# Kernel tuning notes

Hardware: AMD Instinct MI355X
Metric: run time of the kernel (lower is better)

The kernel has to match this reference:

```python
import jax, jax.numpy as jnp
import numpy as np

N_FRAG = 1_000_000
CELL_N = 1000
GENE_N = 500
N_GENES = 5000
H = 100   # hidden dims
E = 100   # embedding dims


def setup_inputs() -> dict:
    key = jax.random.key(0)
    ks = jax.random.split(key, 16)
    coords = jax.random.randint(ks[0], (N_FRAG, 2), 0, 1000, dtype=jnp.int64 if jax.config.jax_enable_x64 else jnp.int32)
    cxg_ix = jnp.sort(jax.random.randint(ks[1], (N_FRAG,), 0, CELL_N * GENE_N))
    gene_ix = jax.random.randint(ks[2], (GENE_N,), 0, N_GENES)
    stdv_in = 1.0 / np.sqrt(2)
    stdv_h = 1.0 / np.sqrt(H)
    u = lambda k, shape, s: jax.random.uniform(k, shape, jnp.float32, -s, s)
    W0 = u(ks[3], (2, H), stdv_in); b0 = u(ks[4], (H,), stdv_in)
    W1 = u(ks[5], (H, H), stdv_h); b1 = u(ks[6], (H,), stdv_h)
    W2 = u(ks[7], (H, H), stdv_h); b2 = u(ks[8], (H,), stdv_h)
    W3 = u(ks[9], (H, E), stdv_h); b3 = u(ks[10], (E,), stdv_h)
    weight1 = u(ks[11], (N_GENES, E), stdv_h / 100.0)  # torch init: stdv/100
    bias1 = jax.random.normal(ks[12], (N_GENES,), jnp.float32)  # mean gene expression
    return {
        "fragment_coordinates": coords,
        "fragment_cellxgene_ix": cxg_ix,
        "cell_n": CELL_N,
        "gene_n": GENE_N,
        "gene_ix": gene_ix,
        "W0": W0, "b0": b0, "W1": W1, "b1": b1,
        "W2": W2, "b2": b2, "W3": W3, "b3": b3,
        "weight1": weight1, "bias1": bias1,
    }


def reference(fragment_coordinates, fragment_cellxgene_ix, cell_n, gene_n, gene_ix,
              W0, b0, W1, b1, W2, b2, W3, b3, weight1, bias1):
    # FragmentEmbedder: 4-layer MLP on scaled coordinates
    x = fragment_coordinates.astype(jnp.float32) / 1000.0          # [F, 2]
    h = jax.nn.relu(x @ W0 + b0)
    h = jax.nn.relu(h @ W1 + b1)
    h = jax.nn.relu(h @ W2 + b2)
    emb = h @ W3 + b3                                              # [F, E]
    # EmbeddingGenePooler: segment-sum into cell x gene bins
    pooled = jax.ops.segment_sum(emb, fragment_cellxgene_ix,
                                 num_segments=cell_n * gene_n)     # [C*G, E]
    cg = pooled.reshape(cell_n, gene_n, -1)                        # [C, G, E]
    # EmbeddingToExpression: gene-specific weighted sum + bias
    out = jnp.einsum('cge,ge->cg', cg, weight1[gene_ix]) + bias1[gene_ix]
    return out
```

## Files before the change

kernel.cpp:

```cpp
#include <hip/hip_runtime.h>
#include <hip/hip_bf16.h>

typedef __attribute__((ext_vector_type(4))) short s16x4;
typedef __attribute__((ext_vector_type(4))) float f32x4;

#define GENE_N     500
#define WG_STRIDE  112
#define WSW_FRAGS  154
#define WG_OFF_BYTES 81920

__device__ __forceinline__ unsigned short f2bf(float x){
  __hip_bfloat16 h = __float2bfloat16(x);
  return *reinterpret_cast<unsigned short*>(&h);
}

__device__ __forceinline__ f32x4 mfma16(s16x4 a, s16x4 b, f32x4 c){
#if __has_builtin(__builtin_amdgcn_mfma_f32_16x16x16bf16_1k)
  return __builtin_amdgcn_mfma_f32_16x16x16bf16_1k(a, b, c, 0, 0, 0);
#else
  asm volatile("v_mfma_f32_16x16x16_bf16 %0, %1, %2, %0"
               : "+v"(c) : "v"(a), "v"(b));
  return c;
#endif
}

__global__ void init_out(const int* __restrict__ gene_ix,
                         const float* __restrict__ bias1,
                         float* __restrict__ out, int n){
  int t = blockIdx.x*blockDim.x + threadIdx.x;
  if (t < n) out[t] = bias1[gene_ix[t % GENE_N]];
}

__global__ void prep_weights(const float* __restrict__ W0, const float* __restrict__ b0,
                             const float* __restrict__ W1, const float* __restrict__ b1,
                             const float* __restrict__ W2, const float* __restrict__ b2,
                             const float* __restrict__ W3, const float* __restrict__ b3,
                             unsigned short* __restrict__ wsW){
  int t = blockIdx.x*blockDim.x + threadIdx.x;
  if (t >= WSW_FRAGS*64) return;
  int fr = t >> 6, lane = t & 63;
  int grp = lane >> 4, row = lane & 15;
  int L, m, kt;
  if (fr < 7){ L = 0; m = fr; kt = 0; }
  else { int r = fr - 7; L = 1 + r/49; r %= 49; m = r/7; kt = r%7; }
  int up = m*16 + row;
  const float* W = (L==0)?W0:(L==1)?W1:(L==2)?W2:W3;
  const float* B = (L==0)?b0:(L==1)?b1:(L==2)?b2:b3;
  #pragma unroll
  for (int i = 0; i < 4; ++i){
    float val = 0.f;
    if (up < 100){
      int k = kt*16 + grp*4 + i;
      if (L == 0){
        if (k < 2)        val = W[k*100 + up];
        else if (k == 2)  val = B[up];
      } else {
        if (k < 100)      val = W[k*100 + up];
        else if (k == 100) val = B[up];
      }
    }
    wsW[t*4 + i] = f2bf(val);
  }
}

__global__ void prep_wg(const int* __restrict__ gene_ix,
                        const float* __restrict__ weight1,
                        float* __restrict__ wg){
  int t = blockIdx.x*blockDim.x + threadIdx.x;
  if (t >= GENE_N*WG_STRIDE) return;
  int g = t / WG_STRIDE, e = t % WG_STRIDE;
  wg[t] = (e < 100) ? weight1[gene_ix[g]*100 + e] : 0.f;
}


__device__ __forceinline__ void mfma_layer(const s16x4* __restrict__ A,
                                           const s16x4* __restrict__ g,
                                           f32x4* __restrict__ acc){
  const f32x4 zero = {0.f,0.f,0.f,0.f};
  #pragma unroll
  for (int m = 0; m < 7; ++m){
    f32x4 a = zero;
    #pragma unroll
    for (int kt = 0; kt < 7; ++kt) a = mfma16(A[m*7 + kt], g[kt], a);
    acc[m] = a;
  }
}

__device__ __forceinline__ void pack_relu(const f32x4* __restrict__ acc,
                                          s16x4* __restrict__ g, int grp){
  #pragma unroll
  for (int m = 0; m < 7; ++m){
    float r0 = fmaxf(acc[m][0], 0.f);
    float r1 = fmaxf(acc[m][1], 0.f);
    float r2 = fmaxf(acc[m][2], 0.f);
    float r3 = fmaxf(acc[m][3], 0.f);
    if (m == 6 && grp == 1) r0 = 1.0f;
    s16x4 v;
    v[0] = (short)f2bf(r0);
    v[1] = (short)f2bf(r1);
    v[2] = (short)f2bf(r2);
    v[3] = (short)f2bf(r3);
    g[m] = v;
  }
}

__device__ __forceinline__ void epi_store(const f32x4* __restrict__ acc,
                                          const float* __restrict__ wg,
                                          int grp, int lane, int f, int nfrag,
                                          int cxgv, float* __restrict__ out){
  int gbin = cxgv % GENE_N;
  const float* wrow = wg + gbin*WG_STRIDE + grp*4;
  float s = 0.f;
  #pragma unroll
  for (int m = 0; m < 7; ++m){
    float4 w = *(const float4*)(wrow + m*16);
    s += acc[m][0]*w.x + acc[m][1]*w.y + acc[m][2]*w.z + acc[m][3]*w.w;
  }
  s += __shfl_xor(s, 16);
  s += __shfl_xor(s, 32);
  if (lane < 16 && f < nfrag) atomicAdd(out + cxgv, s);
}

__device__ __forceinline__ s16x4 build_bx(int2 cd){
  s16x4 v;
  v[0] = (short)f2bf((float)cd.x * 1e-3f);
  v[1] = (short)f2bf((float)cd.y * 1e-3f);
  v[2] = (short)0x3F80;
  v[3] = 0;
  return v;
}

__global__ __launch_bounds__(64, 1)
void frag_mlp_pool(const int* __restrict__ coords, const int* __restrict__ cxg,
                   const unsigned short* __restrict__ wsW,
                   const float* __restrict__ wg,
                   float* __restrict__ out, int nfrag, int ntiles){
  const int lane = threadIdx.x & 63;
  const int grp = lane >> 4, row = lane & 15;
  const s16x4* wf = (const s16x4*)wsW;

  s16x4 A0[7], A1[49], A2[49], A3[49];
  #pragma unroll
  for (int i = 0; i < 7;  ++i) A0[i] = wf[i*64 + lane];
  #pragma unroll
  for (int i = 0; i < 49; ++i) A1[i] = wf[(7   + i)*64 + lane];
  #pragma unroll
  for (int i = 0; i < 49; ++i) A2[i] = wf[(56  + i)*64 + lane];
  #pragma unroll
  for (int i = 0; i < 49; ++i) A3[i] = wf[(105 + i)*64 + lane];

  const f32x4 zero = {0.f,0.f,0.f,0.f};
  const int npairs = (ntiles + 1) >> 1;
  const int lastf = nfrag - 1;

  int p0 = blockIdx.x;
  int fA = p0*32 + row, fB = p0*32 + 16 + row;
  int cA = (fA < nfrag) ? fA : lastf;
  int cB = (fB < nfrag) ? fB : lastf;
  int2 cdA = ((const int2*)coords)[cA];
  int2 cdB = ((const int2*)coords)[cB];
  int  xgA = cxg[cA];
  int  xgB = cxg[cB];

  for (int p = p0; p < npairs; p += gridDim.x){
    int f0 = p*32 + row, f1 = p*32 + 16 + row;
    int2 cd0 = cdA, cd1 = cdB;
    int  xg0 = xgA, xg1 = xgB;

    int pn = p + gridDim.x;
    int fAn = pn*32 + row, fBn = pn*32 + 16 + row;
    int cAn = (fAn < nfrag) ? fAn : lastf;
    int cBn = (fBn < nfrag) ? fBn : lastf;
    cdA = ((const int2*)coords)[cAn];
    cdB = ((const int2*)coords)[cBn];
    xgA = cxg[cAn];
    xgB = cxg[cBn];

    s16x4 bx0 = build_bx(cd0);
    s16x4 bx1 = build_bx(cd1);
    f32x4 acc0[7], acc1[7];
    #pragma unroll
    for (int m = 0; m < 7; ++m) acc0[m] = mfma16(A0[m], bx0, zero);
    #pragma unroll
    for (int m = 0; m < 7; ++m) acc1[m] = mfma16(A0[m], bx1, zero);

    s16x4 g0[7], g1[7];
    pack_relu(acc0, g0, grp);
    mfma_layer(A1, g0, acc0);   pack_relu(acc1, g1, grp);
    mfma_layer(A1, g1, acc1);   pack_relu(acc0, g0, grp);
    mfma_layer(A2, g0, acc0);   pack_relu(acc1, g1, grp);
    mfma_layer(A2, g1, acc1);   pack_relu(acc0, g0, grp);
    mfma_layer(A3, g0, acc0);   pack_relu(acc1, g1, grp);
    mfma_layer(A3, g1, acc1);

    epi_store(acc0, wg, grp, lane, f0, nfrag, xg0, out);
    epi_store(acc1, wg, grp, lane, f1, nfrag, xg1, out);
  }
}

extern "C" void kernel_launch(void* const* d_in, const int* in_sizes, int n_in,
                              void* d_out, int out_size, void* d_ws, size_t ws_size,
                              hipStream_t stream){
  const int* coords  = (const int*)d_in[0];
  const int* cxg     = (const int*)d_in[1];
  const int* gene_ix = (const int*)d_in[4];
  const float* W0 = (const float*)d_in[5];
  const float* b0 = (const float*)d_in[6];
  const float* W1 = (const float*)d_in[7];
  const float* b1 = (const float*)d_in[8];
  const float* W2 = (const float*)d_in[9];
  const float* b2 = (const float*)d_in[10];
  const float* W3 = (const float*)d_in[11];
  const float* b3 = (const float*)d_in[12];
  const float* weight1 = (const float*)d_in[13];
  const float* bias1   = (const float*)d_in[14];

  int nfrag  = in_sizes[1];
  int ntiles = (nfrag + 15) / 16;

  unsigned short* wsW = (unsigned short*)d_ws;
  float* wg = (float*)((char*)d_ws + WG_OFF_BYTES);
  float* out = (float*)d_out;

  hipLaunchKernelGGL(init_out, dim3((out_size + 255)/256), dim3(256), 0, stream,
                     gene_ix, bias1, out, out_size);
  hipLaunchKernelGGL(prep_weights, dim3((WSW_FRAGS*64 + 255)/256), dim3(256), 0, stream,
                     W0, b0, W1, b1, W2, b2, W3, b3, wsW);
  hipLaunchKernelGGL(prep_wg, dim3((GENE_N*WG_STRIDE + 255)/256), dim3(256), 0, stream,
                     gene_ix, weight1, wg);
  hipLaunchKernelGGL(frag_mlp_pool, dim3(1024), dim3(64), 0, stream,
                     coords, cxg, wsW, wg, out, nfrag, ntiles);
}
```

Measured before the change: 181.0 us.

## Use 16x16x32 bf16 MFMA for hidden layers with repacked weight fragments

The three hidden layers now run on the 16x16x32 bf16 MFMA instruction: three double-K ops plus one 16x16x16 op for the tail, replacing seven 16x16x16 ops per output tile. Weights are repacked into 8-element K fragments plus a tail fragment to match. The ReLU-to-bf16 packing now uses bit tricks and byte permutes in place of library conversions. The goal is fewer MFMA issues and cheaper packing per layer. The risks are a changed register-resident weight layout and different rounding behaviour (round-half-up without NaN handling).

```diff
diff --git a/kernel.cpp b/kernel.cpp
--- a/kernel.cpp
+++ b/kernel.cpp
@@ -3,11 +3,15 @@
 
 typedef __attribute__((ext_vector_type(4))) short s16x4;
 typedef __attribute__((ext_vector_type(4))) float f32x4;
+typedef __attribute__((ext_vector_type(8))) unsigned short u16x8;
+typedef __attribute__((ext_vector_type(8))) __bf16 bf16x8;
 
 #define GENE_N     500
 #define WG_STRIDE  112
-#define WSW_FRAGS  154
 #define WG_OFF_BYTES 81920
+#define OFF_B_BYTES 3584
+#define OFF_C_BYTES 68096
+#define NFRAG_TOTAL 91
 
 __device__ __forceinline__ unsigned short f2bf(float x){
   __hip_bfloat16 h = __float2bfloat16(x);
@@ -15,13 +19,11 @@
 }
 
 __device__ __forceinline__ f32x4 mfma16(s16x4 a, s16x4 b, f32x4 c){
-#if __has_builtin(__builtin_amdgcn_mfma_f32_16x16x16bf16_1k)
   return __builtin_amdgcn_mfma_f32_16x16x16bf16_1k(a, b, c, 0, 0, 0);
-#else
-  asm volatile("v_mfma_f32_16x16x16_bf16 %0, %1, %2, %0"
-               : "+v"(c) : "v"(a), "v"(b));
-  return c;
-#endif
+}
+
+__device__ __forceinline__ f32x4 mfma32(bf16x8 a, bf16x8 b, f32x4 c){
+  return __builtin_amdgcn_mfma_f32_16x16x32_bf16(a, b, c, 0, 0, 0);
 }
 
 __global__ void init_out(const int* __restrict__ gene_ix,
@@ -37,29 +39,57 @@
                              const float* __restrict__ W3, const float* __restrict__ b3,
                              unsigned short* __restrict__ wsW){
   int t = blockIdx.x*blockDim.x + threadIdx.x;
-  if (t >= WSW_FRAGS*64) return;
+  if (t >= NFRAG_TOTAL*64) return;
   int fr = t >> 6, lane = t & 63;
   int grp = lane >> 4, row = lane & 15;
-  int L, m, kt;
-  if (fr < 7){ L = 0; m = fr; kt = 0; }
-  else { int r = fr - 7; L = 1 + r/49; r %= 49; m = r/7; kt = r%7; }
-  int up = m*16 + row;
-  const float* W = (L==0)?W0:(L==1)?W1:(L==2)?W2:W3;
-  const float* B = (L==0)?b0:(L==1)?b1:(L==2)?b2:b3;
-  #pragma unroll
-  for (int i = 0; i < 4; ++i){
-    float val = 0.f;
-    if (up < 100){
-      int k = kt*16 + grp*4 + i;
-      if (L == 0){
-        if (k < 2)        val = W[k*100 + up];
-        else if (k == 2)  val = B[up];
-      } else {
-        if (k < 100)      val = W[k*100 + up];
+
+  if (fr < 7){
+    int up = fr*16 + row;
+    unsigned short* dst = wsW + (fr*64 + lane)*4;
+    #pragma unroll
+    for (int i = 0; i < 4; ++i){
+      int k = grp*4 + i;
+      float val = 0.f;
+      if (up < 100){
+        if (k < 2)       val = W0[k*100 + up];
+        else if (k == 2) val = b0[up];
+      }
+      dst[i] = f2bf(val);
+    }
+  } else if (fr < 70){
+    int fb = fr - 7;
+    int L = fb/21, m = (fb%21)/3, q = fb%3;
+    const float* W = (L==0)?W1:(L==1)?W2:W3;
+    const float* B = (L==0)?b1:(L==1)?b2:b3;
+    int up = m*16 + row;
+    unsigned short* dst = wsW + OFF_B_BYTES/2 + (fb*64 + lane)*8;
+    #pragma unroll
+    for (int i = 0; i < 8; ++i){
+      int k = 32*q + ((i < 4) ? (grp*4 + i) : (16 + grp*4 + (i-4)));
+      float val = 0.f;
+      if (up < 100){
+        if (k < 100)       val = W[k*100 + up];
         else if (k == 100) val = B[up];
       }
+      dst[i] = f2bf(val);
     }
-    wsW[t*4 + i] = f2bf(val);
+  } else {
+    int fc = fr - 70;
+    int L = fc/7, m = fc%7;
+    const float* W = (L==0)?W1:(L==1)?W2:W3;
+    const float* B = (L==0)?b1:(L==1)?b2:b3;
+    int up = m*16 + row;
+    unsigned short* dst = wsW + OFF_C_BYTES/2 + (fc*64 + lane)*4;
+    #pragma unroll
+    for (int i = 0; i < 4; ++i){
+      int k = 96 + grp*4 + i;
+      float val = 0.f;
+      if (up < 100){
+        if (k < 100)       val = W[k*100 + up];
+        else if (k == 100) val = B[up];
+      }
+      dst[i] = f2bf(val);
+    }
   }
 }
 
@@ -73,34 +103,47 @@
 }
 
 
-__device__ __forceinline__ void mfma_layer(const s16x4* __restrict__ A,
-                                           const s16x4* __restrict__ g,
-                                           f32x4* __restrict__ acc){
+__device__ __forceinline__ unsigned fbits(float x){ return __builtin_bit_cast(unsigned, x); }
+
+__device__ __forceinline__ void pack_relu2(const f32x4* __restrict__ acc,
+                                           unsigned* __restrict__ pl,
+                                           unsigned* __restrict__ ph, bool selb){
+  #pragma unroll
+  for (int m = 0; m < 7; ++m){
+    unsigned u0 = fbits(fmaxf(acc[m][0], 0.f)) + 0x8000u;
+    unsigned u1 = fbits(fmaxf(acc[m][1], 0.f)) + 0x8000u;
+    unsigned u2 = fbits(fmaxf(acc[m][2], 0.f)) + 0x8000u;
+    unsigned u3 = fbits(fmaxf(acc[m][3], 0.f)) + 0x8000u;
+    unsigned lo = __builtin_amdgcn_perm(u1, u0, 0x07060302u);
+    unsigned hi = __builtin_amdgcn_perm(u3, u2, 0x07060302u);
+    if (m == 6) lo = selb ? ((lo & 0xFFFF0000u) | 0x3F80u) : lo;
+    pl[m] = lo; ph[m] = hi;
+  }
+}
+
+__device__ __forceinline__ bf16x8 catB(unsigned a0, unsigned a1, unsigned b0, unsigned b1){
+  uint4 u; u.x = a0; u.y = a1; u.z = b0; u.w = b1;
+  return __builtin_bit_cast(bf16x8, u);
+}
+
+__device__ __forceinline__ void hidden_layer(const bf16x8* __restrict__ Wd,
+                                             const s16x4* __restrict__ Wt,
+                                             const unsigned* __restrict__ pl,
+                                             const unsigned* __restrict__ ph,
+                                             f32x4* __restrict__ acc){
   const f32x4 zero = {0.f,0.f,0.f,0.f};
+  bf16x8 B0 = catB(pl[0], ph[0], pl[1], ph[1]);
+  bf16x8 B1 = catB(pl[2], ph[2], pl[3], ph[3]);
+  bf16x8 B2 = catB(pl[4], ph[4], pl[5], ph[5]);
+  uint2 t6; t6.x = pl[6]; t6.y = ph[6];
+  s16x4 b6 = __builtin_bit_cast(s16x4, t6);
   #pragma unroll
   for (int m = 0; m < 7; ++m){
-    f32x4 a = zero;
-    #pragma unroll
-    for (int kt = 0; kt < 7; ++kt) a = mfma16(A[m*7 + kt], g[kt], a);
+    f32x4 a = mfma32(Wd[3*m  ], B0, zero);
+    a       = mfma32(Wd[3*m+1], B1, a);
+    a       = mfma32(Wd[3*m+2], B2, a);
+    a       = mfma16(Wt[m],     b6, a);
     acc[m] = a;
-  }
-}
-
-__device__ __forceinline__ void pack_relu(const f32x4* __restrict__ acc,
-                                          s16x4* __restrict__ g, int grp){
-  #pragma unroll
-  for (int m = 0; m < 7; ++m){
-    float r0 = fmaxf(acc[m][0], 0.f);
-    float r1 = fmaxf(acc[m][1], 0.f);
-    float r2 = fmaxf(acc[m][2], 0.f);
-    float r3 = fmaxf(acc[m][3], 0.f);
-    if (m == 6 && grp == 1) r0 = 1.0f;
-    s16x4 v;
-    v[0] = (short)f2bf(r0);
-    v[1] = (short)f2bf(r1);
-    v[2] = (short)f2bf(r2);
-    v[3] = (short)f2bf(r3);
-    g[m] = v;
   }
 }
 
@@ -137,17 +180,29 @@
                    float* __restrict__ out, int nfrag, int ntiles){
   const int lane = threadIdx.x & 63;
   const int grp = lane >> 4, row = lane & 15;
-  const s16x4* wf = (const s16x4*)wsW;
-
-  s16x4 A0[7], A1[49], A2[49], A3[49];
-  #pragma unroll
-  for (int i = 0; i < 7;  ++i) A0[i] = wf[i*64 + lane];
-  #pragma unroll
-  for (int i = 0; i < 49; ++i) A1[i] = wf[(7   + i)*64 + lane];
-  #pragma unroll
-  for (int i = 0; i < 49; ++i) A2[i] = wf[(56  + i)*64 + lane];
-  #pragma unroll
-  for (int i = 0; i < 49; ++i) A3[i] = wf[(105 + i)*64 + lane];
+  const bool selb = (grp == 1);
+
+  const s16x4* wfA = (const s16x4*)wsW;
+  const u16x8* wfB = (const u16x8*)(wsW + OFF_B_BYTES/2);
+  const s16x4* wfC = (const s16x4*)(wsW + OFF_C_BYTES/2);
+
+  s16x4 A0[7];
+  bf16x8 W1d[21], W2d[21], W3d[21];
+  s16x4 W1t[7], W2t[7], W3t[7];
+  #pragma unroll
+  for (int i = 0; i < 7;  ++i) A0[i] = wfA[i*64 + lane];
+  #pragma unroll
+  for (int i = 0; i < 21; ++i) W1d[i] = __builtin_bit_cast(bf16x8, wfB[(i     )*64 + lane]);
+  #pragma unroll
+  for (int i = 0; i < 21; ++i) W2d[i] = __builtin_bit_cast(bf16x8, wfB[(21 + i)*64 + lane]);
+  #pragma unroll
+  for (int i = 0; i < 21; ++i) W3d[i] = __builtin_bit_cast(bf16x8, wfB[(42 + i)*64 + lane]);
+  #pragma unroll
+  for (int i = 0; i < 7;  ++i) W1t[i] = wfC[(i     )*64 + lane];
+  #pragma unroll
+  for (int i = 0; i < 7;  ++i) W2t[i] = wfC[( 7 + i)*64 + lane];
+  #pragma unroll
+  for (int i = 0; i < 7;  ++i) W3t[i] = wfC[(14 + i)*64 + lane];
 
   const f32x4 zero = {0.f,0.f,0.f,0.f};
   const int npairs = (ntiles + 1) >> 1;
@@ -184,14 +239,14 @@
     #pragma unroll
     for (int m = 0; m < 7; ++m) acc1[m] = mfma16(A0[m], bx1, zero);
 
-    s16x4 g0[7], g1[7];
-    pack_relu(acc0, g0, grp);
-    mfma_layer(A1, g0, acc0);   pack_relu(acc1, g1, grp);
-    mfma_layer(A1, g1, acc1);   pack_relu(acc0, g0, grp);
-    mfma_layer(A2, g0, acc0);   pack_relu(acc1, g1, grp);
-    mfma_layer(A2, g1, acc1);   pack_relu(acc0, g0, grp);
-    mfma_layer(A3, g0, acc0);   pack_relu(acc1, g1, grp);
-    mfma_layer(A3, g1, acc1);
+    unsigned pl0[7], ph0[7], pl1[7], ph1[7];
+    pack_relu2(acc0, pl0, ph0, selb);
+    hidden_layer(W1d, W1t, pl0, ph0, acc0);   pack_relu2(acc1, pl1, ph1, selb);
+    hidden_layer(W1d, W1t, pl1, ph1, acc1);   pack_relu2(acc0, pl0, ph0, selb);
+    hidden_layer(W2d, W2t, pl0, ph0, acc0);   pack_relu2(acc1, pl1, ph1, selb);
+    hidden_layer(W2d, W2t, pl1, ph1, acc1);   pack_relu2(acc0, pl0, ph0, selb);
+    hidden_layer(W3d, W3t, pl0, ph0, acc0);   pack_relu2(acc1, pl1, ph1, selb);
+    hidden_layer(W3d, W3t, pl1, ph1, acc1);
 
     epi_store(acc0, wg, grp, lane, f0, nfrag, xg0, out);
     epi_store(acc1, wg, grp, lane, f1, nfrag, xg1, out);
@@ -224,7 +279,7 @@
 
   hipLaunchKernelGGL(init_out, dim3((out_size + 255)/256), dim3(256), 0, stream,
                      gene_ix, bias1, out, out_size);
-  hipLaunchKernelGGL(prep_weights, dim3((WSW_FRAGS*64 + 255)/256), dim3(256), 0, stream,
+  hipLaunchKernelGGL(prep_weights, dim3((NFRAG_TOTAL*64 + 255)/256), dim3(256), 0, stream,
                      W0, b0, W1, b1, W2, b2, W3, b3, wsW);
   hipLaunchKernelGGL(prep_wg, dim3((GENE_N*WG_STRIDE + 255)/256), dim3(256), 0, stream,
                      gene_ix, weight1, wg);
```

After: 172.0 us. -4.9%, faster.
